# Kernel optimization log

Hardware: AMD Instinct MI355X
Metric: run time of the kernel (lower is better)

## Reference

```python
import jax, jax.numpy as jnp
import numpy as np

ITERATIONS = 20
EPSILON = 1.0
UNUSED_SCORE = 1.0


def setup_inputs() -> dict:
    key = jax.random.key(0)
    k1, k2 = jax.random.split(key)
    desc1 = jax.random.normal(k1, (8, 2048, 256), dtype=jnp.float32)
    desc2 = jax.random.normal(k2, (8, 2048, 256), dtype=jnp.float32)
    return {"desc1": desc1, "desc2": desc2}


def _log_scores(desc1, desc2):
    # squared-L2 cost via norms + gemm: [B,N,M]
    n1 = jnp.sum(desc1 * desc1, axis=-1, keepdims=True)            # [B,N,1]
    n2 = jnp.sum(desc2 * desc2, axis=-1, keepdims=True)            # [B,M,1]
    cost = n1 + jnp.swapaxes(n2, -2, -1) - 2.0 * jnp.einsum('bnd,bmd->bnm', desc1, desc2)
    cost = jnp.maximum(cost, 0.0)
    core = -cost / EPSILON                                         # [B,N,M]
    dustbin = jnp.float32(-UNUSED_SCORE / EPSILON)
    return jnp.pad(core, ((0, 0), (0, 1), (0, 1)), constant_values=dustbin)


def reference(desc1, desc2):
    B, N, D = desc1.shape
    M = desc2.shape[1]
    log_scores = _log_scores(desc1, desc2)                         # [B,N+1,M+1]
    log_mu = jnp.concatenate(
        [jnp.zeros((B, N), desc1.dtype),
         jnp.full((B, 1), jnp.log(jnp.float32(M)), desc1.dtype)], axis=1)
    log_nu = jnp.concatenate(
        [jnp.zeros((B, M), desc2.dtype),
         jnp.full((B, 1), jnp.log(jnp.float32(N)), desc2.dtype)], axis=1)

    def body(carry, _):
        u, v = carry
        u = log_mu - jax.nn.logsumexp(log_scores + v[:, None, :], axis=-1)
        v = log_nu - jax.nn.logsumexp(log_scores + u[:, :, None], axis=-2)
        return (u, v), None

    u0 = jnp.zeros_like(log_mu)
    v0 = jnp.zeros_like(log_nu)
    (u, v), _ = jax.lax.scan(body, (u0, v0), None, length=ITERATIONS)
    log_P = log_scores + u[:, :, None] + v[:, None, :]
    return jnp.exp(log_P)
```

## Files before the change

### kernel.cpp

```cpp
#include <hip/hip_runtime.h>
#include <math.h>

#define BB 8
#define NN 2048
#define DD 256
#define NP 2049
#define AVP 2052
#define E1 0.36787944117144233f
#define PADK 40
#define ITERS 20

typedef _Float16 f16;
typedef __attribute__((ext_vector_type(8))) _Float16 f16x8;
typedef __attribute__((ext_vector_type(4))) float f32x4;
typedef __attribute__((ext_vector_type(2))) float f32x2;

#define DEC0(DW) __builtin_amdgcn_cvt_pk_f32_fp8((int)(DW), false)
#define DEC1(DW) __builtin_amdgcn_cvt_pk_f32_fp8((int)(DW), true)

__global__ __launch_bounds__(256) void split_cvt(const float* __restrict__ d1,
                                                 const float* __restrict__ d2,
                                                 f16* __restrict__ A16,
                                                 f16* __restrict__ B16,
                                                 float* __restrict__ n1,
                                                 float* __restrict__ n2) {
    const float* src = blockIdx.z ? d2 : d1;
    f16* dst = blockIdx.z ? B16 : A16;
    float* nn = blockIdx.z ? n2 : n1;
    const int b = blockIdx.y;
    const int row = blockIdx.x * 8 + (threadIdx.x >> 5);
    const int e0 = (threadIdx.x & 31) * 8;
    const size_t base = ((size_t)b * NN + row) * DD + e0;
    f32x4 v0 = *(const f32x4*)(src + base);
    f32x4 v1 = *(const f32x4*)(src + base + 4);
    f16x8 h;
    float s = 0.f;
    #pragma unroll
    for (int e = 0; e < 4; ++e) {
        h[e] = (f16)v0[e]; h[e + 4] = (f16)v1[e];
        s = fmaf(v0[e], v0[e], s);
        s = fmaf(v1[e], v1[e], s);
    }
    *(f16x8*)(dst + base) = h;
    #pragma unroll
    for (int off = 1; off < 32; off <<= 1) s += __shfl_xor(s, off);
    if ((threadIdx.x & 31) == 0) nn[b * NN + row] = s;
}

__global__ __launch_bounds__(512) void gemm128(const f16* __restrict__ A16,
                                               const f16* __restrict__ B16,
                                               const float* __restrict__ n1,
                                               const float* __restrict__ n2,
                                               unsigned char* __restrict__ Kc,
                                               int* __restrict__ flags,
                                               int* __restrict__ zflags,
                                               float* __restrict__ out) {
    __shared__ f16 As[2][128 * PADK];
    __shared__ f16 Bs[2][256 * PADK];
    __shared__ int anyq[2];

    const int b = blockIdx.z;
    const int rt = blockIdx.x, ct = blockIdx.y;
    const int n0 = rt * 128, m0 = ct * 256;
    const int t = threadIdx.x;
    const int wave = t >> 6, lane = t & 63;
    const int wrow = (wave >> 2) * 64;
    const int wcol = (wave & 3) * 64;
    const f16* A  = A16 + ((size_t)b * NN + n0) * DD;
    const f16* Bm = B16 + ((size_t)b * NN + m0) * DD;
    float* ob = out + (size_t)b * NP * NP;

    const int rowA = t >> 2, qk = (t & 3) * 8;
    const int rowB2 = 128 + rowA;
    if (t < 2) anyq[t] = 0;

    f32x4 zero = {0.f, 0.f, 0.f, 0.f};
    f32x4 acc[4][4];
    #pragma unroll
    for (int i = 0; i < 4; ++i)
        #pragma unroll
        for (int j = 0; j < 4; ++j) acc[i][j] = zero;

    const int rb = lane & 15;
    const int kg = (lane >> 4) * 8;

    f16x8 pa  = *(const f16x8*)(A  + (size_t)rowA  * DD + qk);
    f16x8 pb1 = *(const f16x8*)(Bm + (size_t)rowA  * DD + qk);
    f16x8 pb2 = *(const f16x8*)(Bm + (size_t)rowB2 * DD + qk);
    *(f16x8*)&As[0][rowA  * PADK + qk] = pa;
    *(f16x8*)&Bs[0][rowA  * PADK + qk] = pb1;
    *(f16x8*)&Bs[0][rowB2 * PADK + qk] = pb2;
    pa  = *(const f16x8*)(A  + (size_t)rowA  * DD + 32 + qk);
    pb1 = *(const f16x8*)(Bm + (size_t)rowA  * DD + 32 + qk);
    pb2 = *(const f16x8*)(Bm + (size_t)rowB2 * DD + 32 + qk);
    __syncthreads();

    const int pcol = m0 + (t & 31) * 8;
    const int prow0 = n0 + (t >> 5);
    int cur = 0;

    for (int s = 0; s < 8; ++s) {
        f16x8 af[4], bf[4];
        #pragma unroll
        for (int f = 0; f < 4; ++f) {
            af[f] = *(const f16x8*)&As[cur][(wrow + f * 16 + rb) * PADK + kg];
            bf[f] = *(const f16x8*)&Bs[cur][(wcol + f * 16 + rb) * PADK + kg];
        }
        #pragma unroll
        for (int i = 0; i < 4; ++i)
            #pragma unroll
            for (int j = 0; j < 4; ++j)
                acc[i][j] = __builtin_amdgcn_mfma_f32_16x16x32_f16(bf[j], af[i], acc[i][j], 0, 0, 0);

        {
            int row = prow0 + s * 16;
            __builtin_nontemporal_store(zero, (f32x4*)&ob[(size_t)row * NP + pcol]);
            __builtin_nontemporal_store(zero, (f32x4*)&ob[(size_t)row * NP + pcol + 4]);
        }

        if (s < 7) {
            *(f16x8*)&As[cur ^ 1][rowA  * PADK + qk] = pa;
            *(f16x8*)&Bs[cur ^ 1][rowA  * PADK + qk] = pb1;
            *(f16x8*)&Bs[cur ^ 1][rowB2 * PADK + qk] = pb2;
            if (s < 6) {
                int k0 = (s + 2) * 32;
                pa  = *(const f16x8*)(A  + (size_t)rowA  * DD + k0 + qk);
                pb1 = *(const f16x8*)(Bm + (size_t)rowA  * DD + k0 + qk);
                pb2 = *(const f16x8*)(Bm + (size_t)rowB2 * DD + k0 + qk);
            }
        }
        __syncthreads();
        cur ^= 1;
    }

    const int mg = (lane >> 4) * 4;
    float rn_[4];
    f32x4 cn_[4];
    #pragma unroll
    for (int i = 0; i < 4; ++i)
        rn_[i] = n1[b * NN + n0 + wrow + i * 16 + rb];
    #pragma unroll
    for (int j = 0; j < 4; ++j)
        cn_[j] = *(const f32x4*)&n2[b * NN + m0 + wcol + j * 16 + mg];

    int nzany = 0;
    #pragma unroll
    for (int i = 0; i < 4; ++i)
        #pragma unroll
        for (int j = 0; j < 4; ++j) {
            f32x4 a = acc[i][j];
            nzany |= (rn_[i] + cn_[j].x - 2.f * a.x < 7.5f);
            nzany |= (rn_[i] + cn_[j].y - 2.f * a.y < 7.5f);
            nzany |= (rn_[i] + cn_[j].z - 2.f * a.z < 7.5f);
            nzany |= (rn_[i] + cn_[j].w - 2.f * a.w < 7.5f);
        }
    if (nzany) anyq[wcol >> 7] = 1;
    __syncthreads();
    const int anyblk = anyq[0] | anyq[1];

    if (anyblk) {
        #pragma unroll
        for (int i = 0; i < 4; ++i) {
            int n = wrow + i * 16 + rb;
            unsigned char* orow = Kc + ((size_t)b * NN + n0 + n) * NN + m0 + wcol + mg;
            #pragma unroll
            for (int j = 0; j < 4; ++j) {
                f32x4 a = acc[i][j];
                float v0 = __expf(-fmaxf(rn_[i] + cn_[j].x - 2.f * a.x, 0.f));
                float v1 = __expf(-fmaxf(rn_[i] + cn_[j].y - 2.f * a.y, 0.f));
                float v2 = __expf(-fmaxf(rn_[i] + cn_[j].z - 2.f * a.z, 0.f));
                float v3 = __expf(-fmaxf(rn_[i] + cn_[j].w - 2.f * a.w, 0.f));
                int p = __builtin_amdgcn_cvt_pk_fp8_f32(v0, v1, 0, false);
                p = __builtin_amdgcn_cvt_pk_fp8_f32(v2, v3, p, true);
                *(unsigned int*)(orow + j * 16) = (unsigned int)p;
            }
        }
    }
    if (t < 2) flags[b * 256 + rt * 16 + ct * 2 + t] = anyq[t] ? 1 : 0;
    if (t == 0) zflags[b * 128 + rt * 8 + ct] = anyblk ? 0 : 1;
}

__global__ __launch_bounds__(1024) void sinkhorn_iter(
    const unsigned char* __restrict__ Kc,
    const int* __restrict__ flags,
    float* __restrict__ av, float* __restrict__ bv,
    float* __restrict__ out)
{
    const int batch = blockIdx.x;
    const int t = threadIdx.x;
    const int lane = t & 63, w = t >> 6;
    __shared__ float a_sh[NN], b_sh[NN], rs_sh[NN];
    __shared__ float p8[128][9];
    __shared__ float wred[16];
    __shared__ float scal[2];
    __shared__ int flg[256];
    __shared__ int rowNZ[16], colNZ[16], anyNZ;

    if (t < 256) flg[t] = flags[batch * 256 + t];
    if (t == 0) anyNZ = 0;
    __syncthreads();
    if (t < 16) {
        int o = 0;
        #pragma unroll
        for (int j = 0; j < 16; ++j) o |= flg[t * 16 + j];
        rowNZ[t] = o;
        if (o) atomicOr(&anyNZ, 1);
    } else if (t < 32) {
        int j = t - 16, o = 0;
        #pragma unroll
        for (int i = 0; i < 16; ++i) o |= flg[i * 16 + j];
        colNZ[j] = o;
    }
    __syncthreads();
    const unsigned char* Kb = Kc + (size_t)batch * NN * NN;
    float* avb = av + (size_t)batch * AVP;
    float* bvb = bv + (size_t)batch * AVP;
    float* ob = out + (size_t)batch * NP * NP;

    if (!anyNZ) {
        float bMv = 1.f, bcore = 1.f, aNv = 0.f, acore = 0.f;
        for (int it = 0; it < ITERS; ++it) {
            float Sb = 2048.f * bcore + bMv;
            aNv = 2048.f / (E1 * Sb);
            acore = 1.0f / (E1 * bMv);
            float Sa = 2048.f * acore + aNv;
            bcore = 1.0f / (E1 * aNv);
            bMv = 2048.f / (E1 * Sa);
        }
        avb[t] = acore; avb[t + 1024] = acore;
        bvb[t] = bcore; bvb[t + 1024] = bcore;
        if (t == 0) { avb[NN] = aNv; bvb[NN] = bMv; }
        ob[(size_t)t * NP + NN] = acore * E1 * bMv;
        ob[(size_t)(t + 1024) * NP + NN] = acore * E1 * bMv;
        ob[(size_t)NN * NP + t] = aNv * E1 * bcore;
        ob[(size_t)NN * NP + t + 1024] = aNv * E1 * bcore;
        if (t == 0) ob[(size_t)NN * NP + NN] = aNv * E1 * bMv;
        return;
    }

    b_sh[t] = 1.f; b_sh[t + 1024] = 1.f;
    float bMv = 1.f, aNv = 0.f;
    const int r = t >> 3, c8 = (t & 7) * 16;
    __syncthreads();

    for (int it = 0; it < ITERS; ++it) {
        float sb = b_sh[t] + b_sh[t + 1024];
        #pragma unroll
        for (int off = 1; off < 64; off <<= 1) sb += __shfl_xor(sb, off);
        if (lane == 0) wred[w] = sb;
        rs_sh[t] = 0.f; rs_sh[t + 1024] = 0.f;
        __syncthreads();
        if (t == 0) {
            float S = bMv;
            #pragma unroll
            for (int k = 0; k < 16; ++k) S += wred[k];
            scal[0] = 2048.f / (E1 * S);
        }
        __syncthreads();
        aNv = scal[0];

        for (int i = 0; i < 16; ++i) {
            if (!rowNZ[i]) continue;
            float acc = 0.f;
            for (int j = 0; j < 16; ++j) {
                if (!flg[i * 16 + j]) continue;
                const unsigned char* p = Kb + (size_t)(i * 128 + r) * NN + j * 128 + c8;
                uint4 kv = *(const uint4*)p;
                const float* bp = &b_sh[j * 128 + c8];
                unsigned int dwv[4] = {kv.x, kv.y, kv.z, kv.w};
                #pragma unroll
                for (int q = 0; q < 4; ++q) {
                    f32x2 u0 = DEC0(dwv[q]); f32x2 u1 = DEC1(dwv[q]);
                    acc += u0.x * bp[4 * q] + u0.y * bp[4 * q + 1]
                         + u1.x * bp[4 * q + 2] + u1.y * bp[4 * q + 3];
                }
            }
            p8[r][t & 7] = acc;
            __syncthreads();
            if (t < 128) {
                float s = 0.f;
                #pragma unroll
                for (int k = 0; k < 8; ++k) s += p8[t][k];
                rs_sh[i * 128 + t] = s;
            }
            __syncthreads();
        }
        float ebM = E1 * bMv;
        float a0 = 1.0f / (rs_sh[t] + ebM);
        float a1 = 1.0f / (rs_sh[t + 1024] + ebM);
        a_sh[t] = a0; a_sh[t + 1024] = a1;
        float sa = a0 + a1;
        #pragma unroll
        for (int off = 1; off < 64; off <<= 1) sa += __shfl_xor(sa, off);
        if (lane == 0) wred[w] = sa;
        __syncthreads();
        if (t == 0) {
            float S = aNv;
            #pragma unroll
            for (int k = 0; k < 16; ++k) S += wred[k];
            scal[1] = 2048.f / (E1 * S);
        }
        rs_sh[t] = 0.f; rs_sh[t + 1024] = 0.f;
        __syncthreads();

        for (int j = 0; j < 16; ++j) {
            if (!colNZ[j]) continue;
            float acc = 0.f;
            int col = j * 128 + r;
            for (int i = 0; i < 16; ++i) {
                if (!flg[i * 16 + j]) continue;
                #pragma unroll
                for (int e = 0; e < 16; ++e) {
                    int rr2 = i * 128 + c8 + e;
                    f32x2 u = DEC0((unsigned int)Kb[(size_t)rr2 * NN + col]);
                    acc += u.x * a_sh[rr2];
                }
            }
            p8[r][t & 7] = acc;
            __syncthreads();
            if (t < 128) {
                float s = 0.f;
                #pragma unroll
                for (int k = 0; k < 8; ++k) s += p8[t][k];
                rs_sh[j * 128 + t] = s;
            }
            __syncthreads();
        }
        float eaN = E1 * aNv;
        b_sh[t] = 1.0f / (rs_sh[t] + eaN);
        b_sh[t + 1024] = 1.0f / (rs_sh[t + 1024] + eaN);
        bMv = scal[1];
        __syncthreads();
    }
    avb[t] = a_sh[t]; avb[t + 1024] = a_sh[t + 1024];
    bvb[t] = b_sh[t]; bvb[t + 1024] = b_sh[t + 1024];
    if (t == 0) { avb[NN] = aNv; bvb[NN] = bMv; }
    ob[(size_t)t * NP + NN] = a_sh[t] * E1 * bMv;
    ob[(size_t)(t + 1024) * NP + NN] = a_sh[t + 1024] * E1 * bMv;
    ob[(size_t)NN * NP + t] = aNv * E1 * b_sh[t];
    ob[(size_t)NN * NP + t + 1024] = aNv * E1 * b_sh[t + 1024];
    if (t == 0) ob[(size_t)NN * NP + NN] = aNv * E1 * bMv;
}

__global__ __launch_bounds__(1024) void finalize_k(
    const unsigned char* __restrict__ Kc,
    const int* __restrict__ flags,
    const int* __restrict__ zflags,
    const float* __restrict__ av, const float* __restrict__ bv,
    float* __restrict__ out)
{
    const int colhalf = blockIdx.x;
    const int rt = blockIdx.y;
    const int batch = blockIdx.z;
    const int t = threadIdx.x;
    const int tsub = t & 255;
    const int rq = t >> 8;
    const int c0 = colhalf * 1024;
    const int r0 = rt * 128;

    const int jt = colhalf * 8 + (tsub >> 5);
    const int z = zflags[batch * 128 + rt * 8 + (jt >> 1)];
    if (z) return;

    const float* avb = av + (size_t)batch * AVP;
    const float* bvb = bv + (size_t)batch * AVP;
    float* ob = out + (size_t)batch * NP * NP;
    const unsigned char* Kb = Kc + (size_t)batch * NN * NN;
    const int f = flags[batch * 256 + rt * 16 + jt];
    const f32x4 b4 = *(const f32x4*)&bvb[c0 + tsub * 4];

    for (int rr = 0; rr < 32; ++rr) {
        int row = r0 + rr * 4 + rq;
        f32x4 val;
        if (f) {
            float a = avb[row];
            unsigned int kw = *(const unsigned int*)(Kb + (size_t)row * NN + c0 + tsub * 4);
            f32x2 u0 = DEC0(kw), u1 = DEC1(kw);
            val.x = a * u0.x * b4.x; val.y = a * u0.y * b4.y;
            val.z = a * u1.x * b4.z; val.w = a * u1.y * b4.w;
        } else {
            val.x = 0.f; val.y = 0.f; val.z = 0.f; val.w = 0.f;
        }
        __builtin_nontemporal_store(val, (f32x4*)&ob[(size_t)row * NP + c0 + tsub * 4]);
    }
}

extern "C" void kernel_launch(void* const* d_in, const int* in_sizes, int n_in,
                              void* d_out, int out_size, void* d_ws, size_t ws_size,
                              hipStream_t stream) {
    const float* d1 = (const float*)d_in[0];
    const float* d2 = (const float*)d_in[1];
    float* out = (float*)d_out;

    const size_t KCB = (size_t)BB * NN * NN;
    const size_t F16C = (size_t)BB * NN * DD;
    unsigned char* Kc = (unsigned char*)d_ws;
    f16* A16 = (f16*)(Kc + KCB);
    f16* B16 = A16 + F16C;
    int* flags = (int*)(B16 + F16C);
    int* zflags = flags + BB * 256;
    float* av = (float*)(zflags + BB * 128);
    float* bv = av + (size_t)BB * AVP;
    float* n1 = bv + (size_t)BB * AVP;
    float* n2 = n1 + (size_t)BB * NN;

    split_cvt<<<dim3(NN / 8, BB, 2), 256, 0, stream>>>(d1, d2, A16, B16, n1, n2);
    gemm128<<<dim3(16, 8, BB), 512, 0, stream>>>(A16, B16, n1, n2, Kc, flags, zflags, out);
    sinkhorn_iter<<<BB, 1024, 0, stream>>>(Kc, flags, av, bv, out);
    finalize_k<<<dim3(2, 16, BB), 1024, 0, stream>>>(Kc, flags, zflags, av, bv, out);
}
```

Before: 58.95 us.

## Fuse finalize into sinkhorn kernel and zero-fill all output tiles in gemm

Drops the separate finalize kernel. The sinkhorn kernel now writes the nonzero output tiles itself, using the scaling vectors already in shared memory and the per-tile flags. The gemm prologue now zero-fills output at a stride of 128 columns, so every tile starts zeroed and zero tiles no longer need to be written in finalize. This saves one launch and the av/bv round trip. The cost is that the final write is done by only 8 blocks, one per batch, instead of a wide grid, which could limit bandwidth when many tiles are nonzero.

```diff
diff --git a/kernel.cpp b/kernel.cpp
--- a/kernel.cpp
+++ b/kernel.cpp
@@ -95,7 +95,7 @@
     pb2 = *(const f16x8*)(Bm + (size_t)rowB2 * DD + 32 + qk);
     __syncthreads();
 
-    const int pcol = m0 + (t & 31) * 8;
+    const int pc = m0 + (t & 31) * 4;
     const int prow0 = n0 + (t >> 5);
     int cur = 0;
 
@@ -114,8 +114,8 @@
 
         {
             int row = prow0 + s * 16;
-            __builtin_nontemporal_store(zero, (f32x4*)&ob[(size_t)row * NP + pcol]);
-            __builtin_nontemporal_store(zero, (f32x4*)&ob[(size_t)row * NP + pcol + 4]);
+            __builtin_nontemporal_store(zero, (f32x4*)&ob[(size_t)row * NP + pc]);
+            __builtin_nontemporal_store(zero, (f32x4*)&ob[(size_t)row * NP + pc + 128]);
         }
 
         if (s < 7) {
@@ -340,48 +340,31 @@
     ob[(size_t)NN * NP + t] = aNv * E1 * b_sh[t];
     ob[(size_t)NN * NP + t + 1024] = aNv * E1 * b_sh[t + 1024];
     if (t == 0) ob[(size_t)NN * NP + NN] = aNv * E1 * bMv;
-}
-
-__global__ __launch_bounds__(1024) void finalize_k(
-    const unsigned char* __restrict__ Kc,
-    const int* __restrict__ flags,
-    const int* __restrict__ zflags,
-    const float* __restrict__ av, const float* __restrict__ bv,
-    float* __restrict__ out)
-{
-    const int colhalf = blockIdx.x;
-    const int rt = blockIdx.y;
-    const int batch = blockIdx.z;
-    const int t = threadIdx.x;
-    const int tsub = t & 255;
-    const int rq = t >> 8;
-    const int c0 = colhalf * 1024;
-    const int r0 = rt * 128;
-
-    const int jt = colhalf * 8 + (tsub >> 5);
-    const int z = zflags[batch * 128 + rt * 8 + (jt >> 1)];
-    if (z) return;
-
-    const float* avb = av + (size_t)batch * AVP;
-    const float* bvb = bv + (size_t)batch * AVP;
-    float* ob = out + (size_t)batch * NP * NP;
-    const unsigned char* Kb = Kc + (size_t)batch * NN * NN;
-    const int f = flags[batch * 256 + rt * 16 + jt];
-    const f32x4 b4 = *(const f32x4*)&bvb[c0 + tsub * 4];
-
-    for (int rr = 0; rr < 32; ++rr) {
-        int row = r0 + rr * 4 + rq;
-        f32x4 val;
-        if (f) {
-            float a = avb[row];
-            unsigned int kw = *(const unsigned int*)(Kb + (size_t)row * NN + c0 + tsub * 4);
-            f32x2 u0 = DEC0(kw), u1 = DEC1(kw);
-            val.x = a * u0.x * b4.x; val.y = a * u0.y * b4.y;
-            val.z = a * u1.x * b4.z; val.w = a * u1.y * b4.w;
-        } else {
-            val.x = 0.f; val.y = 0.f; val.z = 0.f; val.w = 0.f;
-        }
-        __builtin_nontemporal_store(val, (f32x4*)&ob[(size_t)row * NP + c0 + tsub * 4]);
+
+    const int fr = t >> 3;
+    const int fc = (t & 7) * 16;
+    for (int i = 0; i < 16; ++i) {
+        if (!rowNZ[i]) continue;
+        for (int j = 0; j < 16; ++j) {
+            if (!flg[i * 16 + j]) continue;
+            int row = i * 128 + fr;
+            int col = j * 128 + fc;
+            float a = a_sh[row];
+            const unsigned char* kp = Kb + (size_t)row * NN + col;
+            uint4 kv = *(const uint4*)kp;
+            unsigned int dwv[4] = {kv.x, kv.y, kv.z, kv.w};
+            float* op = ob + (size_t)row * NP + col;
+            #pragma unroll
+            for (int q = 0; q < 4; ++q) {
+                f32x2 u0 = DEC0(dwv[q]); f32x2 u1 = DEC1(dwv[q]);
+                f32x4 val;
+                val.x = a * u0.x * b_sh[col + 4 * q];
+                val.y = a * u0.y * b_sh[col + 4 * q + 1];
+                val.z = a * u1.x * b_sh[col + 4 * q + 2];
+                val.w = a * u1.y * b_sh[col + 4 * q + 3];
+                *(f32x4*)(op + 4 * q) = val;
+            }
+        }
     }
 }
 
@@ -407,5 +390,4 @@
     split_cvt<<<dim3(NN / 8, BB, 2), 256, 0, stream>>>(d1, d2, A16, B16, n1, n2);
     gemm128<<<dim3(16, 8, BB), 512, 0, stream>>>(A16, B16, n1, n2, Kc, flags, zflags, out);
     sinkhorn_iter<<<BB, 1024, 0, stream>>>(Kc, flags, av, bv, out);
-    finalize_k<<<dim3(2, 16, BB), 1024, 0, stream>>>(Kc, flags, zflags, av, bv, out);
 }
```

New measurement: 53.18 us (median of 2 runs). -9.8%, faster.
